# Kernel tuning notes

Hardware: AMD Instinct MI355X
Metric: run time of the kernel (lower is better)

Reference implementation:

```python
import jax, jax.numpy as jnp
import numpy as np

B, CIN, COUT, H, W = 8, 128, 128, 64, 64

# kernel-grid base offsets (dy, dx), row-major k = kh*3 + kw, matching torch base_offset-1
BASE = jnp.array([[-1, -1], [-1, 0], [-1, 1],
                  [0, -1], [0, 0], [0, 1],
                  [1, -1], [1, 0], [1, 1]], dtype=jnp.float32)  # [9,2]
CORNER = jnp.array([1, 0, 1, 0, 0, 0, 1, 0, 1], dtype=jnp.float32)  # mask1 per kernel tap
EDGE = jnp.array([0, 1, 0, 1, 0, 1, 0, 1, 0], dtype=jnp.float32)    # mask2 per kernel tap


def conv3x3(x, w, b=None):
    out = jax.lax.conv_general_dilated(
        x, w, window_strides=(1, 1), padding=((1, 1), (1, 1)),
        dimension_numbers=('NCHW', 'OIHW', 'NCHW'))
    if b is not None:
        out = out + b[None, :, None, None]
    return out


def bilinear_sample(x, py, px):
    Bv, C, Hin, Win = x.shape
    y0 = jnp.floor(py)
    x0 = jnp.floor(px)
    wy = py - y0
    wx = px - x0
    y0i = y0.astype(jnp.int32)
    x0i = x0.astype(jnp.int32)
    xf = x.reshape(Bv, C, Hin * Win)

    def corner(yi, xi):
        valid = ((yi >= 0) & (yi < Hin) & (xi >= 0) & (xi < Win)).astype(x.dtype)
        idx = jnp.clip(yi, 0, Hin - 1) * Win + jnp.clip(xi, 0, Win - 1)  # [B,K,Ho,Wo]
        g = jax.vmap(lambda xb, ib: xb[:, ib])(xf, idx)  # [B,C,K,Ho,Wo]
        return g * valid[:, None]

    v00 = corner(y0i, x0i)
    v01 = corner(y0i, x0i + 1)
    v10 = corner(y0i + 1, x0i)
    v11 = corner(y0i + 1, x0i + 1)
    wy = wy[:, None]
    wx = wx[:, None]
    return (v00 * (1 - wy) * (1 - wx) + v01 * (1 - wy) * wx
            + v10 * wy * (1 - wx) + v11 * wy * wx)


def setup_inputs() -> dict:
    key = jax.random.key(0)
    k1, k2, k3 = jax.random.split(key, 3)
    x = jax.random.normal(k1, (B, CIN, H, W), dtype=jnp.float32)
    # small offset-conv weights keep predicted offsets in a realistic sub-pixel range
    w_off = jax.random.normal(k2, (5, CIN, 3, 3), dtype=jnp.float32) * 0.02
    b_off = jnp.zeros((5,), dtype=jnp.float32)
    w = jax.random.normal(k3, (COUT, CIN, 3, 3), dtype=jnp.float32) * (1.0 / np.sqrt(CIN * 9))
    b = jnp.zeros((COUT,), dtype=jnp.float32)
    return {"x": x, "w_off": w_off, "b_off": b_off, "w": w, "b": b}


def reference(x, w_off, b_off, w, b):
    off = conv3x3(x, w_off, b_off)          # [B,5,H,W]
    scale1 = jax.nn.relu(off[:, 2:3]) + 1.0  # corner scale [B,1,H,W]
    scale2 = jax.nn.relu(off[:, 3:4]) + 1.0  # edge scale   [B,1,H,W]
    shift = off[:, :2]                       # equivariant shift vector [B,2,H,W]

    # per-tap scale; center tap gets 0 but its base offset is (0,0) anyway
    scale_k = CORNER[None, :, None, None] * scale1 + EDGE[None, :, None, None] * scale2  # [B,9,H,W]
    # deform offset = scaled_base - base + shift = base*(scale-1) + shift
    delta = BASE[None, :, :, None, None] * (scale_k - 1.0)[:, :, None] + shift[:, None]  # [B,9,2,H,W]

    hs = jnp.arange(H, dtype=x.dtype)
    ws = jnp.arange(W, dtype=x.dtype)
    # sampling positions: p0 + base_k + offset_k (stride=1, pad=1)
    py = hs[None, None, :, None] + BASE[None, :, 0, None, None] + delta[:, :, 0]  # [B,9,H,W]
    px = ws[None, None, None, :] + BASE[None, :, 1, None, None] + delta[:, :, 1]

    sampled = bilinear_sample(x, py, px)  # [B,CIN,9,H,W]
    out = jnp.einsum('bckhw,ock->bohw', sampled, w.reshape(COUT, CIN, 9))
    return out + b[None, :, None, None]
```

## Files before the change

kernel.cpp:

```cpp
#include <hip/hip_runtime.h>

#define Wd 64
#define Hd 64
#define HWp 4096
#define CIN_ 128
#define COUT_ 128

typedef _Float16 f16;
typedef _Float16 h2    __attribute__((ext_vector_type(2)));
typedef _Float16 f16x8 __attribute__((ext_vector_type(8)));
typedef float f32x4    __attribute__((ext_vector_type(4)));

__device__ inline ushort f2h(float f) {
    f16 h = (f16)f;
    return __builtin_bit_cast(ushort, h);
}
__device__ inline h2 gb(const int4& g, int d) {
    return __builtin_bit_cast(h2, (&g.x)[d]);
}
__device__ inline h2 dup(float f) {
    f16 h = (f16)f;
    h2 r; r[0] = h; r[1] = h;
    return r;
}
struct H8 { h2 r[4]; };

__global__ __launch_bounds__(256) void prep_offsets_kernel(
    const float* __restrict__ x, const float* __restrict__ w,
    const float* __restrict__ w_off, const float* __restrict__ b_off,
    ushort* __restrict__ xt, ushort* __restrict__ w_t2,
    float4* __restrict__ der)
{
    __shared__ char smem[34816];
    int blk = blockIdx.x;
    int t = threadIdx.x;

    if (blk < 256) {
        ushort* tile = (ushort*)smem;
        int b = blk >> 5, yx0 = (blk & 31) << 7;
        const float* xb = x + (size_t)b * CIN_ * HWp + yx0;
        int lanelo = t & 31, grp = t >> 5;
        #pragma unroll
        for (int i = 0; i < 4; i++) {
            int cbase = i * 32 + grp * 4;
            float4 v0 = *(const float4*)(xb + (size_t)(cbase + 0) * HWp + lanelo * 4);
            float4 v1 = *(const float4*)(xb + (size_t)(cbase + 1) * HWp + lanelo * 4);
            float4 v2 = *(const float4*)(xb + (size_t)(cbase + 2) * HWp + lanelo * 4);
            float4 v3 = *(const float4*)(xb + (size_t)(cbase + 3) * HWp + lanelo * 4);
            ushort4 u;
            u.x = f2h(v0.x); u.y = f2h(v1.x); u.z = f2h(v2.x); u.w = f2h(v3.x);
            *(ushort4*)&tile[(lanelo * 4 + 0) * 136 + cbase] = u;
            u.x = f2h(v0.y); u.y = f2h(v1.y); u.z = f2h(v2.y); u.w = f2h(v3.y);
            *(ushort4*)&tile[(lanelo * 4 + 1) * 136 + cbase] = u;
            u.x = f2h(v0.z); u.y = f2h(v1.z); u.z = f2h(v2.z); u.w = f2h(v3.z);
            *(ushort4*)&tile[(lanelo * 4 + 2) * 136 + cbase] = u;
            u.x = f2h(v0.w); u.y = f2h(v1.w); u.z = f2h(v2.w); u.w = f2h(v3.w);
            *(ushort4*)&tile[(lanelo * 4 + 3) * 136 + cbase] = u;
        }
        __syncthreads();
        ushort* dst = xt + ((size_t)b * HWp + yx0) * CIN_;
        int c8 = (t & 15) * 8, yxg = t >> 4;
        #pragma unroll
        for (int i = 0; i < 8; i++) {
            int yxl = i * 16 + yxg;
            int4 v = *(int4*)&tile[yxl * 136 + c8];
            *(int4*)(dst + (size_t)yxl * CIN_ + c8) = v;
        }
    } else if (blk < 832) {
        int i = (blk - 256) * 256 + t;
        int j    = i & 7;
        int lane = (i >> 3) & 63;
        int ii   = (i >> 9) & 3;
        int wm   = (i >> 11) & 1;
        int s    = i >> 12;
        int o = wm * 64 + ii * 16 + (lane & 15);
        int c = (s & 3) * 32 + (lane >> 4) * 8 + j;
        int k = s >> 2;
        w_t2[i] = f2h(w[o * 1152 + c * 9 + k]);
    } else {
        float* wl   = (float*)smem;
        float* part = (float*)(smem + 18432);
        int blk2 = blk - 832;
        int b = blk2 >> 6;
        int h = blk2 & 63;

        for (int i = t; i < 4608; i += 256) {
            int j = i / 1152;
            int r = i - j * 1152;
            wl[r * 4 + j] = w_off[i];
        }
        __syncthreads();

        int pi = t & 63, cc = t >> 6;
        const float* xb = x + (size_t)(b * CIN_ + cc * 32) * HWp;

        int idx9[9];
        float msk9[9];
        #pragma unroll
        for (int dy = 0; dy < 3; dy++) {
            int hy = h + dy - 1;
            int hyc = min(max(hy, 0), Hd - 1);
            bool vr = (hy >= 0) && (hy < Hd);
            #pragma unroll
            for (int dx = 0; dx < 3; dx++) {
                int wx = pi + dx - 1;
                int wxc = min(max(wx, 0), Wd - 1);
                bool v = vr && (wx >= 0) && (wx < Wd);
                idx9[dy * 3 + dx] = hyc * Wd + wxc;
                msk9[dy * 3 + dx] = v ? 1.0f : 0.0f;
            }
        }

        float o0 = 0.f, o1 = 0.f, o2 = 0.f, o3 = 0.f;
        #pragma unroll 2
        for (int c = 0; c < 32; c++) {
            const float* xp = xb + c * HWp;
            const float* wc = &wl[(cc * 32 + c) * 36];
            float xv[9];
            #pragma unroll
            for (int tp = 0; tp < 9; tp++) xv[tp] = xp[idx9[tp]] * msk9[tp];
            #pragma unroll
            for (int tp = 0; tp < 9; tp++) {
                float4 wj = *(const float4*)&wc[tp * 4];
                o0 += xv[tp] * wj.x; o1 += xv[tp] * wj.y;
                o2 += xv[tp] * wj.z; o3 += xv[tp] * wj.w;
            }
        }
        part[t * 4 + 0] = o0;
        part[t * 4 + 1] = o1;
        part[t * 4 + 2] = o2;
        part[t * 4 + 3] = o3;
        __syncthreads();

        if (t < 64) {
            float s0 = b_off[0], s1 = b_off[1], s2 = b_off[2], s3 = b_off[3];
            #pragma unroll
            for (int q = 0; q < 4; q++) {
                s0 += part[(q * 64 + t) * 4 + 0];
                s1 += part[(q * 64 + t) * 4 + 1];
                s2 += part[(q * 64 + t) * 4 + 2];
                s3 += part[(q * 64 + t) * 4 + 3];
            }
            float4 d;
            d.x = s0;
            d.y = s1;
            d.z = fmaxf(s2, 0.f) + 1.f;
            d.w = fmaxf(s3, 0.f) + 1.f;
            der[(size_t)b * HWp + h * Wd + t] = d;
        }
    }
}

__global__ __launch_bounds__(512, 1) void deform_gemm_mfma(
    const ushort* __restrict__ xt, const ushort* __restrict__ w_t2,
    const float* __restrict__ bias, const float4* __restrict__ der,
    float* __restrict__ out)
{
    __shared__ ushort A_lds[2][2][4096];
    __shared__ ushort S_lds[2][2][128 * 40];

    int t = threadIdx.x;
    int b = blockIdx.x >> 5;
    int rp = blockIdx.x & 31;
    int p0 = rp << 7;
    const ushort* xtb = xt + (size_t)b * HWp * CIN_;

    int p  = t >> 2;
    int c8 = (t & 3) << 3;

    int wv = t >> 6, lane = t & 63;
    int wm = wv & 1, ns = wv >> 1;
    int lm = lane & 15, lq = lane >> 4;

    f32x4 acc[4][2] = {};

    int pg = p0 + p;
    float fh = (float)(pg >> 6), fp = (float)(pg & 63);
    float4 dv = der[(size_t)b * HWp + pg];

    const ushort* cbp[4];

    auto computeMeta = [&](int k, h2 (&cw)[4]) {
        int ky = (k * 11) >> 5;
        int kx = k - ky * 3;
        float by = (float)(ky - 1), bx = (float)(kx - 1);
        bool corner = (ky != 1) && (kx != 1);
        bool edge = (ky != 1) ^ (kx != 1);
        float sk = corner ? dv.z : (edge ? dv.w : 0.0f);
        float py = fh + by * sk + dv.x;
        float px = fp + bx * sk + dv.y;
        float y0f = floorf(py), x0f = floorf(px);
        float wy = py - y0f, wx = px - x0f;
        int y0 = (int)y0f, x0 = (int)x0f;
        int y1 = y0 + 1, x1 = x0 + 1;
        float vy0 = (y0 >= 0 && y0 < Hd) ? 1.f : 0.f;
        float vy1 = (y1 >= 0 && y1 < Hd) ? 1.f : 0.f;
        float vx0 = (x0 >= 0 && x0 < Wd) ? 1.f : 0.f;
        float vx1 = (x1 >= 0 && x1 < Wd) ? 1.f : 0.f;
        int cy0 = min(max(y0, 0), Hd - 1), cy1 = min(max(y1, 0), Hd - 1);
        int cx0 = min(max(x0, 0), Wd - 1), cx1 = min(max(x1, 0), Wd - 1);
        cbp[0] = xtb + (cy0 * Wd + cx0) * CIN_ + c8;
        cbp[1] = xtb + (cy0 * Wd + cx1) * CIN_ + c8;
        cbp[2] = xtb + (cy1 * Wd + cx0) * CIN_ + c8;
        cbp[3] = xtb + (cy1 * Wd + cx1) * CIN_ + c8;
        cw[0] = dup((1.f - wy) * (1.f - wx) * vy0 * vx0);
        cw[1] = dup((1.f - wy) * wx * vy0 * vx1);
        cw[2] = dup(wy * (1.f - wx) * vy1 * vx0);
        cw[3] = dup(wy * wx * vy1 * vx1);
    };

    auto stageA = [&](int buf, int st) {
        const ushort* src = w_t2 + (size_t)st * 8192;
        #pragma unroll
        for (int cc = 0; cc < 2; cc++) {
            const ushort* g = src + cc * 4096 + wv * 512 + lane * 8;
            ushort* l = &A_lds[buf][cc][wv * 512];
            __builtin_amdgcn_global_load_lds(
                (const __attribute__((address_space(1))) unsigned int*)g,
                (__attribute__((address_space(3))) unsigned int*)l, 16, 0, 0);
        }
    };

    auto issue = [&](int st, int4 (&G)[2][4]) {
        #pragma unroll
        for (int cc = 0; cc < 2; cc++) {
            int q = (2 * st + cc) & 3;
            #pragma unroll
            for (int r = 0; r < 4; r++)
                G[cc][r] = *(const int4*)(cbp[r] + q * 32);
        }
    };
    auto commitS = [&](int buf, const int4 (&G)[2][4], const h2 (&cw)[4]) {
        #pragma unroll
        for (int cc = 0; cc < 2; cc++) {
            H8 tmp;
            #pragma unroll
            for (int d = 0; d < 4; d++) {
                h2 r = gb(G[cc][0], d) * cw[0];
                r = gb(G[cc][1], d) * cw[1] + r;
                r = gb(G[cc][2], d) * cw[2] + r;
                r = gb(G[cc][3], d) * cw[3] + r;
                tmp.r[d] = r;
            }
            *(int4*)&S_lds[buf][cc][p * 40 + c8] = __builtin_bit_cast(int4, tmp);
        }
    };
    auto mfmaSec = [&](int cur) {
        #pragma unroll
        for (int cc = 0; cc < 2; cc++) {
            f16x8 af[4], bfr[2];
            #pragma unroll
            for (int i = 0; i < 4; i++)
                af[i] = *(const f16x8*)&A_lds[cur][cc][(wm * 4 + i) * 512 + lane * 8];
            #pragma unroll
            for (int f = 0; f < 2; f++)
                bfr[f] = *(const f16x8*)&S_lds[cur][cc][(ns * 32 + f * 16 + lm) * 40 + lq * 8];
            #pragma unroll
            for (int i = 0; i < 4; i++)
                #pragma unroll
                for (int f = 0; f < 2; f++)
                    acc[i][f] = __builtin_amdgcn_mfma_f32_16x16x32_f16(
                        af[i], bfr[f], acc[i][f], 0, 0, 0);
        }
    };

    int4 GA[2][4], GB[2][4];
    h2 cwA[4], cwB[4];

    computeMeta(0, cwA);
    stageA(0, 0);
    __builtin_amdgcn_sched_barrier(0);
    issue(0, GA);
    commitS(0, GA, cwA);
    issue(1, GB);
    asm volatile("s_waitcnt vmcnt(8) lgkmcnt(0)" ::: "memory");
    __builtin_amdgcn_s_barrier();
    __builtin_amdgcn_sched_barrier(0);

#define BODY(ST, GC, GI, CWC, DOMETA, CWI)                                   \
    {                                                                        \
        int cur_ = (ST) & 1, nb_ = cur_ ^ 1;                                 \
        if ((ST) + 1 < 18) stageA(nb_, (ST) + 1);                            \
        __builtin_amdgcn_sched_barrier(0);                                   \
        if ((ST) + 2 < 18) {                                                 \
            if (DOMETA) computeMeta(((ST) + 2) >> 1, CWI);                   \
            issue((ST) + 2, GI);                                             \
        }                                                                    \
        mfmaSec(cur_);                                                       \
        if ((ST) + 1 < 18) commitS(nb_, GC, CWC);                            \
        if ((ST) + 2 < 18) {                                                 \
            asm volatile("s_waitcnt vmcnt(8) lgkmcnt(0)" ::: "memory");      \
        } else {                                                             \
            asm volatile("s_waitcnt vmcnt(0) lgkmcnt(0)" ::: "memory");      \
        }                                                                    \
        __builtin_amdgcn_s_barrier();                                        \
        __builtin_amdgcn_sched_barrier(0);                                   \
    }

    for (int su = 0; su < 4; su++) {
        int st = su << 2;
        BODY(st,     GB, GA, cwA, 1, cwB);
        BODY(st + 1, GA, GB, cwB, 0, cwB);
        BODY(st + 2, GB, GA, cwB, 1, cwA);
        BODY(st + 3, GA, GB, cwA, 0, cwA);
    }
    BODY(16, GB, GA, cwA, 0, cwA);
    BODY(17, GA, GB, cwA, 0, cwA);
#undef BODY

    #pragma unroll
    for (int i = 0; i < 4; i++) {
        #pragma unroll
        for (int r = 0; r < 4; r++) {
            int o = wm * 64 + i * 16 + lq * 4 + r;
            float bv = bias[o];
            float* orow = out + (size_t)(b * COUT_ + o) * HWp + p0 + ns * 32 + lm;
            #pragma unroll
            for (int f = 0; f < 2; f++)
                orow[f * 16] = acc[i][f][r] + bv;
        }
    }
}

extern "C" void kernel_launch(void* const* d_in, const int* in_sizes, int n_in,
                              void* d_out, int out_size, void* d_ws, size_t ws_size,
                              hipStream_t stream) {
    const float* x     = (const float*)d_in[0];
    const float* w_off = (const float*)d_in[1];
    const float* b_off = (const float*)d_in[2];
    const float* w     = (const float*)d_in[3];
    const float* bias  = (const float*)d_in[4];
    float* out = (float*)d_out;

    char* ws = (char*)d_ws;
    ushort* xt   = (ushort*)ws;
    ushort* w_t2 = (ushort*)(ws + 8388608);
    float4* der  = (float4*)(ws + 8683520);

    prep_offsets_kernel<<<1344, 256, 0, stream>>>(x, w, w_off, b_off,
                                                  xt, w_t2, der);
    deform_gemm_mfma<<<256, 512, 0, stream>>>(xt, w_t2, bias, der, out);
}
```

Before: 116.1 us.

## Precompute bilinear sampling metadata into LDS once per block and reorder grid

```diff
diff --git a/kernel.cpp b/kernel.cpp
--- a/kernel.cpp
+++ b/kernel.cpp
@@ -112,7 +112,7 @@
         }
 
         float o0 = 0.f, o1 = 0.f, o2 = 0.f, o3 = 0.f;
-        #pragma unroll 2
+        #pragma unroll 4
         for (int c = 0; c < 32; c++) {
             const float* xp = xb + c * HWp;
             const float* wc = &wl[(cc * 32 + c) * 36];
@@ -158,15 +158,18 @@
 {
     __shared__ ushort A_lds[2][2][4096];
     __shared__ ushort S_lds[2][2][128 * 40];
+    __shared__ int4 MI[9][128];
+    __shared__ int4 MW[9][128];
 
     int t = threadIdx.x;
-    int b = blockIdx.x >> 5;
-    int rp = blockIdx.x & 31;
+    int b = blockIdx.x & 7;
+    int rp = blockIdx.x >> 3;
     int p0 = rp << 7;
-    const ushort* xtb = xt + (size_t)b * HWp * CIN_;
+    const char* xtb = (const char*)(xt + (size_t)b * HWp * CIN_);
 
     int p  = t >> 2;
     int c8 = (t & 3) << 3;
+    int c8b = c8 * 2;
 
     int wv = t >> 6, lane = t & 63;
     int wm = wv & 1, ns = wv >> 1;
@@ -174,40 +177,46 @@
 
     f32x4 acc[4][2] = {};
 
-    int pg = p0 + p;
-    float fh = (float)(pg >> 6), fp = (float)(pg & 63);
-    float4 dv = der[(size_t)b * HWp + pg];
-
-    const ushort* cbp[4];
-
-    auto computeMeta = [&](int k, h2 (&cw)[4]) {
-        int ky = (k * 11) >> 5;
-        int kx = k - ky * 3;
-        float by = (float)(ky - 1), bx = (float)(kx - 1);
-        bool corner = (ky != 1) && (kx != 1);
-        bool edge = (ky != 1) ^ (kx != 1);
-        float sk = corner ? dv.z : (edge ? dv.w : 0.0f);
-        float py = fh + by * sk + dv.x;
-        float px = fp + bx * sk + dv.y;
-        float y0f = floorf(py), x0f = floorf(px);
-        float wy = py - y0f, wx = px - x0f;
-        int y0 = (int)y0f, x0 = (int)x0f;
-        int y1 = y0 + 1, x1 = x0 + 1;
-        float vy0 = (y0 >= 0 && y0 < Hd) ? 1.f : 0.f;
-        float vy1 = (y1 >= 0 && y1 < Hd) ? 1.f : 0.f;
-        float vx0 = (x0 >= 0 && x0 < Wd) ? 1.f : 0.f;
-        float vx1 = (x1 >= 0 && x1 < Wd) ? 1.f : 0.f;
-        int cy0 = min(max(y0, 0), Hd - 1), cy1 = min(max(y1, 0), Hd - 1);
-        int cx0 = min(max(x0, 0), Wd - 1), cx1 = min(max(x1, 0), Wd - 1);
-        cbp[0] = xtb + (cy0 * Wd + cx0) * CIN_ + c8;
-        cbp[1] = xtb + (cy0 * Wd + cx1) * CIN_ + c8;
-        cbp[2] = xtb + (cy1 * Wd + cx0) * CIN_ + c8;
-        cbp[3] = xtb + (cy1 * Wd + cx1) * CIN_ + c8;
-        cw[0] = dup((1.f - wy) * (1.f - wx) * vy0 * vx0);
-        cw[1] = dup((1.f - wy) * wx * vy0 * vx1);
-        cw[2] = dup(wy * (1.f - wx) * vy1 * vx0);
-        cw[3] = dup(wy * wx * vy1 * vx1);
-    };
+    {
+        int pg = p0 + p;
+        float fh = (float)(pg >> 6), fp = (float)(pg & 63);
+        float4 dv = der[(size_t)b * HWp + pg];
+        for (int k = (t & 3); k < 9; k += 4) {
+            int ky = (k * 11) >> 5;
+            int kx = k - ky * 3;
+            float by = (float)(ky - 1), bx = (float)(kx - 1);
+            bool corner = (ky != 1) && (kx != 1);
+            bool edge = (ky != 1) ^ (kx != 1);
+            float sk = corner ? dv.z : (edge ? dv.w : 0.0f);
+            float py = fh + by * sk + dv.x;
+            float px = fp + bx * sk + dv.y;
+            float y0f = floorf(py), x0f = floorf(px);
+            float wy = py - y0f, wx = px - x0f;
+            int y0 = (int)y0f, x0 = (int)x0f;
+            int y1 = y0 + 1, x1 = x0 + 1;
+            float vy0 = (y0 >= 0 && y0 < Hd) ? 1.f : 0.f;
+            float vy1 = (y1 >= 0 && y1 < Hd) ? 1.f : 0.f;
+            float vx0 = (x0 >= 0 && x0 < Wd) ? 1.f : 0.f;
+            float vx1 = (x1 >= 0 && x1 < Wd) ? 1.f : 0.f;
+            int cy0 = min(max(y0, 0), Hd - 1), cy1 = min(max(y1, 0), Hd - 1);
+            int cx0 = min(max(x0, 0), Wd - 1), cx1 = min(max(x1, 0), Wd - 1);
+            int4 ii;
+            ii.x = (cy0 * Wd + cx0) << 8;
+            ii.y = (cy0 * Wd + cx1) << 8;
+            ii.z = (cy1 * Wd + cx0) << 8;
+            ii.w = (cy1 * Wd + cx1) << 8;
+            MI[k][p] = ii;
+            H8 hw;
+            hw.r[0] = dup((1.f - wy) * (1.f - wx) * vy0 * vx0);
+            hw.r[1] = dup((1.f - wy) * wx * vy0 * vx1);
+            hw.r[2] = dup(wy * (1.f - wx) * vy1 * vx0);
+            hw.r[3] = dup(wy * wx * vy1 * vx1);
+            MW[k][p] = __builtin_bit_cast(int4, hw);
+        }
+    }
+    __syncthreads();
+
+    int vo0, vo1, vo2, vo3;
 
     auto stageA = [&](int buf, int st) {
         const ushort* src = w_t2 + (size_t)st * 8192;
@@ -225,21 +234,22 @@
         #pragma unroll
         for (int cc = 0; cc < 2; cc++) {
             int q = (2 * st + cc) & 3;
-            #pragma unroll
-            for (int r = 0; r < 4; r++)
-                G[cc][r] = *(const int4*)(cbp[r] + q * 32);
+            G[cc][0] = *(const int4*)(xtb + (vo0 + q * 64));
+            G[cc][1] = *(const int4*)(xtb + (vo1 + q * 64));
+            G[cc][2] = *(const int4*)(xtb + (vo2 + q * 64));
+            G[cc][3] = *(const int4*)(xtb + (vo3 + q * 64));
         }
     };
-    auto commitS = [&](int buf, const int4 (&G)[2][4], const h2 (&cw)[4]) {
+    auto commitS = [&](int buf, const int4 (&G)[2][4], const H8& cw) {
         #pragma unroll
         for (int cc = 0; cc < 2; cc++) {
             H8 tmp;
             #pragma unroll
             for (int d = 0; d < 4; d++) {
-                h2 r = gb(G[cc][0], d) * cw[0];
-                r = gb(G[cc][1], d) * cw[1] + r;
-                r = gb(G[cc][2], d) * cw[2] + r;
-                r = gb(G[cc][3], d) * cw[3] + r;
+                h2 r = gb(G[cc][0], d) * cw.r[0];
+                r = gb(G[cc][1], d) * cw.r[1] + r;
+                r = gb(G[cc][2], d) * cw.r[2] + r;
+                r = gb(G[cc][3], d) * cw.r[3] + r;
                 tmp.r[d] = r;
             }
             *(int4*)&S_lds[buf][cc][p * 40 + c8] = __builtin_bit_cast(int4, tmp);
@@ -265,28 +275,43 @@
     };
 
     int4 GA[2][4], GB[2][4];
-    h2 cwA[4], cwB[4];
-
-    computeMeta(0, cwA);
+    H8 cwA, cwB;
+    int4 idxN;
+
     stageA(0, 0);
     __builtin_amdgcn_sched_barrier(0);
+    {
+        int4 i0 = MI[0][p];
+        vo0 = i0.x + c8b; vo1 = i0.y + c8b; vo2 = i0.z + c8b; vo3 = i0.w + c8b;
+    }
     issue(0, GA);
+    cwA = __builtin_bit_cast(H8, MW[0][p]);
     commitS(0, GA, cwA);
     issue(1, GB);
+    idxN = MI[1][p];
     asm volatile("s_waitcnt vmcnt(8) lgkmcnt(0)" ::: "memory");
     __builtin_amdgcn_s_barrier();
     __builtin_amdgcn_sched_barrier(0);
 
-#define BODY(ST, GC, GI, CWC, DOMETA, CWI)                                   \
+#define BODY(ST, GC, GI, CWC, CWR, DORD)                                     \
     {                                                                        \
         int cur_ = (ST) & 1, nb_ = cur_ ^ 1;                                 \
         if ((ST) + 1 < 18) stageA(nb_, (ST) + 1);                            \
         __builtin_amdgcn_sched_barrier(0);                                   \
         if ((ST) + 2 < 18) {                                                 \
-            if (DOMETA) computeMeta(((ST) + 2) >> 1, CWI);                   \
+            if (DORD) {                                                      \
+                vo0 = idxN.x + c8b; vo1 = idxN.y + c8b;                      \
+                vo2 = idxN.z + c8b; vo3 = idxN.w + c8b;                      \
+            }                                                                \
             issue((ST) + 2, GI);                                             \
         }                                                                    \
+        if (DORD) {                                                          \
+            idxN = MI[min(((ST) >> 1) + 2, 8)][p];                           \
+            CWR = __builtin_bit_cast(H8, MW[min(((ST) >> 1) + 1, 8)][p]);    \
+        }                                                                    \
+        __builtin_amdgcn_s_setprio(1);                                       \
         mfmaSec(cur_);                                                       \
+        __builtin_amdgcn_s_setprio(0);                                       \
         if ((ST) + 1 < 18) commitS(nb_, GC, CWC);                            \
         if ((ST) + 2 < 18) {                                                 \
             asm volatile("s_waitcnt vmcnt(8) lgkmcnt(0)" ::: "memory");      \
@@ -299,13 +324,13 @@
 
     for (int su = 0; su < 4; su++) {
         int st = su << 2;
-        BODY(st,     GB, GA, cwA, 1, cwB);
-        BODY(st + 1, GA, GB, cwB, 0, cwB);
-        BODY(st + 2, GB, GA, cwB, 1, cwA);
-        BODY(st + 3, GA, GB, cwA, 0, cwA);
-    }
-    BODY(16, GB, GA, cwA, 0, cwA);
-    BODY(17, GA, GB, cwA, 0, cwA);
+        BODY(st,     GB, GA, cwA, cwB, 1);
+        BODY(st + 1, GA, GB, cwB, cwB, 0);
+        BODY(st + 2, GB, GA, cwB, cwA, 1);
+        BODY(st + 3, GA, GB, cwA, cwA, 0);
+    }
+    BODY(16, GB, GA, cwA, cwB, 1);
+    BODY(17, GA, GB, cwB, cwB, 0);
 #undef BODY
 
     #pragma unroll
@@ -317,7 +342,7 @@
             float* orow = out + (size_t)(b * COUT_ + o) * HWp + p0 + ns * 32 + lm;
             #pragma unroll
             for (int f = 0; f < 2; f++)
-                orow[f * 16] = acc[i][f][r] + bv;
+                __builtin_nontemporal_store(acc[i][f][r] + bv, &orow[f * 16]);
         }
     }
 }
```

Result: no change. 116.0 us (-0.1%).
